# Performance work log

Measured on AMD Instinct MI355X. Metric: run time of the kernel, lower is better.

## Reference

```python
import jax, jax.numpy as jnp
import numpy as np

GAMMA = 0.99
NUM_QUANTILES = 50
STEP_TYPE_LAST = 2
HUBER_DELTA = 1.0

T, B, Q = 128, 512, NUM_QUANTILES


def setup_inputs() -> dict:
    key = jax.random.key(0)
    k1, k2, k3, k4, k5 = jax.random.split(key, 5)
    return {
        "reward": jax.random.normal(k1, (T, B), dtype=jnp.float32),
        "step_type": jax.random.randint(k2, (T, B), 0, 3, dtype=jnp.int32),
        "discount": jax.random.uniform(k3, (T, B), dtype=jnp.float32),
        "value": jax.random.normal(k4, (T, B, Q), dtype=jnp.float32),
        "target_value": jax.random.normal(k5, (T, B, Q), dtype=jnp.float32),
    }


def discounted_return(rewards, values, step_types, discounts):
    """alf value_ops.discounted_return: backward-in-time recurrence.

    rewards/step_types/discounts: [T, B]; values: [T, B, Q].
    Returns [T-1, B, Q]. rets[T-1]=values[T-1];
    rets[t] = is_last[t]*values[t] + (1-is_last[t])*(discounts[t+1]*rets[t+1] + rewards[t+1]).
    """
    is_last = (step_types == STEP_TYPE_LAST).astype(values.dtype)[..., None]  # [T,B,1]
    r = rewards[..., None]    # [T,B,1]
    d = discounts[..., None]  # [T,B,1]

    def step(carry, xs):
        is_last_t, v_t, r_tp1, d_tp1 = xs
        acc = carry * d_tp1 + r_tp1
        ret = is_last_t * v_t + (1.0 - is_last_t) * acc
        return ret, ret

    init = values[-1]
    xs = (is_last[:-1], values[:-1], r[1:], d[1:])
    _, rets = jax.lax.scan(step, init, xs, reverse=True)
    return rets  # [T-1, B, Q]


def huber(x):
    ax = jnp.abs(x)
    return jnp.where(ax <= HUBER_DELTA, 0.5 * x * x, HUBER_DELTA * (ax - 0.5 * HUBER_DELTA))


def reference(reward, step_type, discount, value, target_value):
    # td_lambda == 1.0 -> full discounted return (computed with no grad / detached)
    returns = jax.lax.stop_gradient(
        discounted_return(reward, target_value, step_type, discount * GAMMA))  # [T-1,B,Q]
    v = value[:-1]  # [T-1,B,Q]

    q = returns.shape[-1]
    tau = (jnp.arange(q, dtype=value.dtype) + 0.5) / q  # [Q] cdf midpoints

    # diff[..., i, j] = target_quantile_i - estimated_quantile_j
    diff = returns[..., :, None] - v[..., None, :]  # [T-1,B,Qt,Qe]
    weight = jnp.abs(tau - (jax.lax.stop_gradient(diff) < 0).astype(diff.dtype))
    loss = weight * huber(diff)
    # sum_over_quantiles=True: mean over target quantiles, sum over estimate quantiles
    loss = loss.mean(axis=-2).sum(axis=-1)  # [T-1,B]
    # tensor_extend_zero: append a zero row for the last time step -> [T,B]
    loss = jnp.concatenate([loss, jnp.zeros_like(loss[-1:])], axis=0)
    return loss
```

## Files before the change

kernel.cpp:

```cpp
#include <hip/hip_runtime.h>

#define GAMMA 0.99f
constexpr int T_DIM = 128;
constexpr int B_DIM = 512;
constexpr int Q_DIM = 50;
constexpr int NROW  = (T_DIM - 1) * B_DIM;
constexpr int SLOT  = 52;
constexpr int R_BLK = 20;
constexpr int KEEP  = -1;
constexpr int GRID_LOSS = (NROW + R_BLK - 1) / R_BLK;

__global__ void __launch_bounds__(128) coeff_kernel(
    const float* __restrict__ reward,
    const int*   __restrict__ step_type,
    const float* __restrict__ discount,
    float* __restrict__ alpha,
    float* __restrict__ beta,
    int*   __restrict__ anchor,
    float* __restrict__ out) {
  __shared__ float sp[128], sqa[128], sqb[128];
  __shared__ int   snv[128];
  const int t = threadIdx.x;
  const int b = blockIdx.x;

  float p, qa, qb; int nv;
  if (t < T_DIM - 1) {
    const bool  last = (step_type[t * B_DIM + b] == 2);
    const float d    = GAMMA * discount[(t + 1) * B_DIM + b];
    const float r    = reward[(t + 1) * B_DIM + b];
    p  = last ? 0.0f : d;
    qa = last ? 1.0f : 0.0f;
    qb = last ? 0.0f : r;
    nv = last ? t    : KEEP;
  } else {
    p = 1.0f; qa = 0.0f; qb = 0.0f; nv = KEEP;
    out[(T_DIM - 1) * B_DIM + b] = 0.0f;
  }
  sp[t] = p; sqa[t] = qa; sqb[t] = qb; snv[t] = nv;
  __syncthreads();

#pragma unroll
  for (int off = 1; off < 128; off <<= 1) {
    const bool act = (t + off) < 128;
    float p2 = 1.0f, qa2 = 0.0f, qb2 = 0.0f; int nv2 = KEEP;
    if (act) { p2 = sp[t+off]; qa2 = sqa[t+off]; qb2 = sqb[t+off]; nv2 = snv[t+off]; }
    __syncthreads();
    if (act) {
      qa = fmaf(p, qa2, qa);
      qb = fmaf(p, qb2, qb);
      p  = p * p2;
      nv = (nv == KEEP) ? nv2 : nv;
      sp[t] = p; sqa[t] = qa; sqb[t] = qb; snv[t] = nv;
    }
    __syncthreads();
  }

  if (t < T_DIM - 1) {
    const int row = (b << 7) + t;
    alpha[row]  = p + qa;
    beta[row]   = qb;
    anchor[row] = (nv == KEEP) ? (T_DIM - 1) : nv;
  }
}

__global__ void __launch_bounds__(256) loss_kernel(
    const float* __restrict__ value,
    const float* __restrict__ tv,
    const float* __restrict__ alpha,
    const float* __restrict__ beta,
    const int*   __restrict__ anchor,
    float*       __restrict__ out) {
  __shared__ __align__(16) float sret[R_BLK * SLOT];
  __shared__ float pacc[R_BLK * SLOT];

  const int tid = threadIdx.x;
  const int r0  = blockIdx.x * R_BLK;

  for (int e = tid; e < R_BLK * Q_DIM; e += 256) {
    const int lr  = e / Q_DIM;
    const int i   = e - lr * Q_DIM;
    const int row = r0 + lr;
    float rv = 0.0f;
    if (row < NROW) {
      const int b  = row & (B_DIM - 1);
      const int t  = row >> 9;
      const int ci = (b << 7) + t;
      const int n  = anchor[ci];
      rv = fmaf(alpha[ci], tv[(n * B_DIM + b) * Q_DIM + i], beta[ci]);
    }
    sret[lr * SLOT + i] = rv;
  }
  __syncthreads();

  const bool act   = tid < 5 * Q_DIM;
  const int  r_off = tid / Q_DIM;
  const int  j     = tid - r_off * Q_DIM;
  const float tm05 = ((float)j + 0.5f) * (1.0f / Q_DIM) - 0.5f;

  if (act) {
#pragma unroll
    for (int rb = 0; rb < 4; ++rb) {
      const int lr = rb * 5 + r_off;
      const float* rp = &sret[lr * SLOT];
      const float v = value[(r0 + rb * 5) * Q_DIM + tid];

      float s = 0.0f;
      auto pair = [&](float reti) {
        const float d  = reti - v;
        const float c  = __builtin_amdgcn_fmed3f(d, -1.0f, 1.0f);
        const float u  = fmaf(-0.5f, fabsf(c), fabsf(d));
        const float in = fmaf(0.5f, fabsf(c), tm05 * c);
        s = fmaf(u, in, s);
      };
#pragma unroll
      for (int i0 = 0; i0 < 48; i0 += 4) {
        const float4 rr = *reinterpret_cast<const float4*>(rp + i0);
        pair(rr.x); pair(rr.y); pair(rr.z); pair(rr.w);
      }
      {
        const float2 rr = *reinterpret_cast<const float2*>(rp + 48);
        pair(rr.x); pair(rr.y);
      }
      pacc[lr * SLOT + j] = s;
    }
  }
  __syncthreads();

  const int w    = tid >> 6;
  const int lane = tid & 63;
#pragma unroll
  for (int k = 0; k < 5; ++k) {
    const int lr   = w * 5 + k;
    const int grow = r0 + lr;
    float x = (lane < Q_DIM) ? pacc[lr * SLOT + lane] : 0.0f;
#pragma unroll
    for (int off = 32; off > 0; off >>= 1)
      x += __shfl_xor(x, off, 64);
    if (lane == 0 && grow < NROW)
      out[grow] = x * (1.0f / Q_DIM);
  }
}

extern "C" void kernel_launch(void* const* d_in, const int* in_sizes, int n_in,
                              void* d_out, int out_size, void* d_ws, size_t ws_size,
                              hipStream_t stream) {
  const float* reward       = (const float*)d_in[0];
  const int*   step_type    = (const int*)  d_in[1];
  const float* discount     = (const float*)d_in[2];
  const float* value        = (const float*)d_in[3];
  const float* target_value = (const float*)d_in[4];
  float* out = (float*)d_out;

  float* alpha  = (float*)d_ws;
  float* beta   = alpha + B_DIM * 128;
  int*   anchor = (int*)(beta + B_DIM * 128);

  coeff_kernel<<<B_DIM, 128, 0, stream>>>(reward, step_type, discount,
                                          alpha, beta, anchor, out);

  loss_kernel<<<GRID_LOSS, 256, 0, stream>>>(value, target_value,
                                             alpha, beta, anchor, out);
}
```

Baseline: 105.2 us.

## Compute two estimate quantiles per thread and factor tau weight out of inner loop

Each thread now handles estimate quantiles j and j+25 over two row groups instead of one quantile over four row groups. This halves the shared-memory reads of the return values per pair. The pinball-Huber term is rewritten as two accumulators, e*c and e*|c| with e = d - 0.5c, so the tau weighting is applied once after the loop and the per-pair work drops by an instruction. The final wave reduction shrinks to 25 lanes. The cost is more live registers per thread and a different floating-point summation order.

```diff
diff --git a/kernel.cpp b/kernel.cpp
--- a/kernel.cpp
+++ b/kernel.cpp
@@ -6,6 +6,7 @@
 constexpr int Q_DIM = 50;
 constexpr int NROW  = (T_DIM - 1) * B_DIM;
 constexpr int SLOT  = 52;
+constexpr int PACC  = 26;
 constexpr int R_BLK = 20;
 constexpr int KEEP  = -1;
 constexpr int GRID_LOSS = (NROW + R_BLK - 1) / R_BLK;
@@ -71,7 +72,7 @@
     const int*   __restrict__ anchor,
     float*       __restrict__ out) {
   __shared__ __align__(16) float sret[R_BLK * SLOT];
-  __shared__ float pacc[R_BLK * SLOT];
+  __shared__ float pacc[R_BLK * PACC];
 
   const int tid = threadIdx.x;
   const int r0  = blockIdx.x * R_BLK;
@@ -92,25 +93,39 @@
   }
   __syncthreads();
 
-  const bool act   = tid < 5 * Q_DIM;
-  const int  r_off = tid / Q_DIM;
-  const int  j     = tid - r_off * Q_DIM;
-  const float tm05 = ((float)j + 0.5f) * (1.0f / Q_DIM) - 0.5f;
+  const bool act   = tid < 250;
+  const int  r_off = tid / 25;
+  const int  jh    = tid - r_off * 25;
+  const float ta   = ((float)jh + 0.5f) * (1.0f / Q_DIM) - 0.5f;
+  const float tb   = ta + 0.5f;
 
   if (act) {
+    const int row0 = r0 + r_off;
+    const int row1 = row0 + 10;
+    const float va0 = value[row0 * Q_DIM + jh];
+    const float vb0 = value[row0 * Q_DIM + jh + 25];
+    const float va1 = value[row1 * Q_DIM + jh];
+    const float vb1 = value[row1 * Q_DIM + jh + 25];
+
 #pragma unroll
-    for (int rb = 0; rb < 4; ++rb) {
-      const int lr = rb * 5 + r_off;
+    for (int rb = 0; rb < 2; ++rb) {
+      const int lr = rb * 10 + r_off;
       const float* rp = &sret[lr * SLOT];
-      const float v = value[(r0 + rb * 5) * Q_DIM + tid];
+      const float va = rb ? va1 : va0;
+      const float vb = rb ? vb1 : vb0;
 
-      float s = 0.0f;
+      float s1a = 0.0f, s2a = 0.0f, s1b = 0.0f, s2b = 0.0f;
       auto pair = [&](float reti) {
-        const float d  = reti - v;
-        const float c  = __builtin_amdgcn_fmed3f(d, -1.0f, 1.0f);
-        const float u  = fmaf(-0.5f, fabsf(c), fabsf(d));
-        const float in = fmaf(0.5f, fabsf(c), tm05 * c);
-        s = fmaf(u, in, s);
+        const float da = reti - va;
+        const float ca = __builtin_amdgcn_fmed3f(da, -1.0f, 1.0f);
+        const float ea = fmaf(-0.5f, ca, da);
+        s1a = fmaf(ea, ca, s1a);
+        s2a = fmaf(ea, fabsf(ca), s2a);
+        const float db = reti - vb;
+        const float cb = __builtin_amdgcn_fmed3f(db, -1.0f, 1.0f);
+        const float eb = fmaf(-0.5f, cb, db);
+        s1b = fmaf(eb, cb, s1b);
+        s2b = fmaf(eb, fabsf(cb), s2b);
       };
 #pragma unroll
       for (int i0 = 0; i0 < 48; i0 += 4) {
@@ -121,7 +136,8 @@
         const float2 rr = *reinterpret_cast<const float2*>(rp + 48);
         pair(rr.x); pair(rr.y);
       }
-      pacc[lr * SLOT + j] = s;
+      pacc[lr * PACC + jh] =
+          fmaf(ta, s2a, 0.5f * s1a) + fmaf(tb, s2b, 0.5f * s1b);
     }
   }
   __syncthreads();
@@ -132,9 +148,9 @@
   for (int k = 0; k < 5; ++k) {
     const int lr   = w * 5 + k;
     const int grow = r0 + lr;
-    float x = (lane < Q_DIM) ? pacc[lr * SLOT + lane] : 0.0f;
+    float x = (lane < 25) ? pacc[lr * PACC + lane] : 0.0f;
 #pragma unroll
-    for (int off = 32; off > 0; off >>= 1)
+    for (int off = 16; off > 0; off >>= 1)
       x += __shfl_xor(x, off, 64);
     if (lane == 0 && grow < NROW)
       out[grow] = x * (1.0f / Q_DIM);
```

Measured after the change: 102.5 us. 2.5% less time.
